# Optimization experiments

Hardware: AMD Instinct MI355X
Metric: run time of the kernel (lower is better)

Reference implementation:

```python
import jax, jax.numpy as jnp
import numpy as np

EPS = 1e-5


def setup_inputs() -> dict:
    key = jax.random.key(0)
    ks = jax.random.split(key, 14)
    N, C, H, W, D = 2048, 512, 4, 4, 64
    inp = {
        "x": jax.random.normal(ks[0], (N, C, H, W), jnp.float32),
        "W123": jax.random.normal(ks[1], (3, D, C), jnp.float32) * 0.05,
        "b123": jax.random.normal(ks[2], (3, D), jnp.float32) * 0.05,
        "g123": jax.random.uniform(ks[3], (3, D), jnp.float32, 0.5, 1.5),
        "be123": jax.random.normal(ks[4], (3, D), jnp.float32) * 0.05,
        "m123": jax.random.normal(ks[5], (3, D), jnp.float32) * 0.05,
        "v123": jax.random.uniform(ks[6], (3, D), jnp.float32, 0.5, 1.5),
        "W4": jax.random.normal(ks[7], (C, D), jnp.float32) * 0.05,
        "b4": jax.random.normal(ks[8], (C,), jnp.float32) * 0.05,
        "g4": jax.random.uniform(ks[9], (C,), jnp.float32, 0.5, 1.5),
        "be4": jax.random.normal(ks[10], (C,), jnp.float32) * 0.05,
        "m4": jax.random.normal(ks[11], (C,), jnp.float32) * 0.05,
        "v4": jax.random.uniform(ks[12], (C,), jnp.float32, 0.5, 1.5),
    }
    return inp


def reference(x, W123, b123, g123, be123, m123, v123, W4, b4, g4, be4, m4, v4):
    N, C, H, W = x.shape
    D = W123.shape[1]
    # three parallel 1x1 stride-2 conv branches == strided slice + channel GEMM
    xs = x[:, :, ::2, ::2]                                 # (N, C, H/2, W/2)
    proj = jnp.einsum('nchw,koc->knohw', xs, W123)         # (3, N, D, H/2, W/2)
    bcast = lambda p: p[:, None, :, None, None]
    bn = (proj + bcast(b123) - bcast(m123)) * (bcast(g123) / jnp.sqrt(bcast(v123) + EPS)) + bcast(be123)
    act = jax.nn.relu(bn)                                  # (3, N, D, h, w)
    L = act.shape[-2] * act.shape[-1]
    q = act[0].reshape(N, D, L).transpose(0, 2, 1)         # (N, L, D)
    k = act[1].reshape(N, D, L)                            # (N, D, L)
    v = act[2].reshape(N, D, L).transpose(0, 2, 1)         # (N, L, D)
    attn = jax.nn.softmax(jnp.einsum('nld,ndm->nlm', q, k), axis=2)  # (N, L, L)
    att = jnp.einsum('nlm,nmd->nld', attn, v).transpose(0, 2, 1)     # (N, D, L)
    att = att.reshape(N, D, W, -1)                         # (N, D, W, L//W)
    # conv2: 1x1 conv D->C + BN (no ReLU)
    out2 = jnp.einsum('ndhw,cd->nchw', att, W4) + b4[None, :, None, None]
    cb = lambda p: p[None, :, None, None]
    bn2 = (out2 - cb(m4)) * (cb(g4) / jnp.sqrt(cb(v4) + EPS)) + cb(be4)
    return x + bn2                                         # broadcasts (N,C,4,1) -> (N,C,4,4)
```

## Files before the change

kernel.cpp:

```cpp
#include <hip/hip_runtime.h>
#include <hip/hip_bf16.h>
#include <math.h>

#define EPS 1e-5f

typedef __attribute__((ext_vector_type(8))) short bf8_t;
typedef __attribute__((ext_vector_type(4))) float f4_t;

static __device__ __forceinline__ unsigned short f2b(float f) {
    __hip_bfloat16 h = __float2bfloat16(f);
    return *reinterpret_cast<unsigned short*>(&h);
}


__global__ __launch_bounds__(256) void k0_prep(
    const float* __restrict__ W123, const float* __restrict__ W4,
    const float* __restrict__ b123, const float* __restrict__ g123,
    const float* __restrict__ be123, const float* __restrict__ m123, const float* __restrict__ v123,
    const float* __restrict__ b4, const float* __restrict__ g4,
    const float* __restrict__ be4, const float* __restrict__ m4, const float* __restrict__ v4,
    unsigned short* __restrict__ w1b, unsigned short* __restrict__ w4b,
    float* __restrict__ bn1s, float* __restrict__ bn1h,
    float* __restrict__ bn2s, float* __restrict__ bn2h)
{
    const int bid = blockIdx.x, tid = threadIdx.x;
    if (bid == 64) {
        if (tid < 192) {
            float s = g123[tid] * rsqrtf(v123[tid] + EPS);
            bn1s[tid] = s;
            bn1h[tid] = be123[tid] + (b123[tid] - m123[tid]) * s;
        }
        for (int c = tid; c < 512; c += 256) {
            float s = g4[c] * rsqrtf(v4[c] + EPS);
            bn2s[c] = s;
            bn2h[c] = be4[c] + (b4[c] - m4[c]) * s;
        }
        return;
    }
    const int f = bid * 256 + tid;
    const float* src;
    unsigned short* dst;
    if (f < 12288) {
        int mt = f >> 10, ks = (f >> 6) & 15, lane = f & 63;
        int row = mt * 16 + (lane & 15);
        int k0  = ks * 32 + ((lane >> 4) << 3);
        src = W123 + row * 512 + k0;
        dst = w1b + f * 8;
    } else {
        int f2 = f - 12288;
        int mt = f2 >> 7, ks = (f2 >> 6) & 1, lane = f2 & 63;
        int row = mt * 16 + (lane & 15);
        int k0  = ks * 32 + ((lane >> 4) << 3);
        src = W4 + row * 64 + k0;
        dst = w4b + f2 * 8;
    }
    float4 a = *(const float4*)src;
    float4 b = *(const float4*)(src + 4);
    union { unsigned short u[8]; uint4 v; } o;
    o.u[0]=f2b(a.x); o.u[1]=f2b(a.y); o.u[2]=f2b(a.z); o.u[3]=f2b(a.w);
    o.u[4]=f2b(b.x); o.u[5]=f2b(b.y); o.u[6]=f2b(b.z); o.u[7]=f2b(b.w);
    *(uint4*)dst = o.v;
}

__global__ __launch_bounds__(256) void k1_mfma(
    const float* __restrict__ x,
    const unsigned short* __restrict__ w1b,
    const unsigned short* __restrict__ w4b,
    const float* __restrict__ bn1s, const float* __restrict__ bn1h,
    const float* __restrict__ bn2s, const float* __restrict__ bn2h,
    float* __restrict__ bn2g)
{
    __shared__ unsigned short Bxs[16][536];
    __shared__ float actL[192][17];
    __shared__ float smx[4][17];
    __shared__ unsigned short B2[16][72];
    __shared__ float C2T[16][524];

    const int tid = threadIdx.x;
    const int lane = tid & 63, w = tid >> 6;
    const int n0 = blockIdx.x * 4;

    #pragma unroll
    for (int it = 0; it < 8; ++it) {
        int i = it * 256 + tid;
        int s = i >> 9, c = i & 511;
        const float* xp = x + (size_t)(n0 + s) * 8192 + c * 16;
        float4 a = *(const float4*)xp;
        float4 b = *(const float4*)(xp + 8);
        Bxs[s * 4 + 0][c] = f2b(a.x);
        Bxs[s * 4 + 1][c] = f2b(a.z);
        Bxs[s * 4 + 2][c] = f2b(b.x);
        Bxs[s * 4 + 3][c] = f2b(b.z);
    }
    __syncthreads();

    {
        f4_t acc[3] = {};
        const bf8_t* Af = (const bf8_t*)w1b;
        const int col = lane & 15, kg = (lane >> 4) << 3;
        for (int ks = 0; ks < 16; ++ks) {
            bf8_t bf = *(const bf8_t*)&Bxs[col][ks * 32 + kg];
            #pragma unroll
            for (int mi = 0; mi < 3; ++mi) {
                int mt = w * 3 + mi;
                bf8_t af = Af[(mt * 16 + ks) * 64 + lane];
                acc[mi] = __builtin_amdgcn_mfma_f32_16x16x32_bf16(af, bf, acc[mi], 0, 0, 0);
            }
        }
        #pragma unroll
        for (int mi = 0; mi < 3; ++mi) {
            int rbase = (w * 3 + mi) * 16 + ((lane >> 4) << 2);
            #pragma unroll
            for (int r = 0; r < 4; ++r) {
                int row = rbase + r;
                float v = acc[mi][r] * bn1s[row] + bn1h[row];
                actL[row][col] = fmaxf(v, 0.f);
            }
        }
    }
    __syncthreads();

    if (tid < 128) {
        int s = tid >> 5, l = (tid >> 3) & 3, m = (tid >> 1) & 3, dg = tid & 1;
        float part = 0.f;
        #pragma unroll 8
        for (int k = 0; k < 32; ++k) {
            int d = dg * 32 + k;
            part += actL[d][s * 4 + l] * actL[64 + d][s * 4 + m];
        }
        part += __shfl_xor(part, 1);
        if (dg == 0) smx[s][l * 4 + m] = part;
    }
    __syncthreads();

    if (tid < 16) {
        int s = tid >> 2, l = tid & 3;
        float s0 = smx[s][l*4+0], s1 = smx[s][l*4+1], s2 = smx[s][l*4+2], s3 = smx[s][l*4+3];
        float mx = fmaxf(fmaxf(s0, s1), fmaxf(s2, s3));
        float e0 = expf(s0-mx), e1 = expf(s1-mx), e2 = expf(s2-mx), e3 = expf(s3-mx);
        float inv = 1.f / (e0 + e1 + e2 + e3);
        smx[s][l*4+0] = e0*inv; smx[s][l*4+1] = e1*inv;
        smx[s][l*4+2] = e2*inv; smx[s][l*4+3] = e3*inv;
    }
    __syncthreads();

    if (tid < 128) {
        int s = tid >> 5, l = (tid >> 3) & 3, d0 = (tid & 7) * 8;
        float p0 = smx[s][l*4+0], p1 = smx[s][l*4+1], p2 = smx[s][l*4+2], p3 = smx[s][l*4+3];
        #pragma unroll
        for (int j = 0; j < 8; ++j) {
            int d = d0 + j;
            float sum = p0 * actL[128+d][s*4+0] + p1 * actL[128+d][s*4+1]
                      + p2 * actL[128+d][s*4+2] + p3 * actL[128+d][s*4+3];
            B2[s * 4 + l][d] = f2b(sum);
        }
    }
    __syncthreads();

    {
        const bf8_t* A2f = (const bf8_t*)w4b;
        const int col = lane & 15, kg = (lane >> 4) << 3;
        f4_t acc2[8] = {};
        #pragma unroll
        for (int ks = 0; ks < 2; ++ks) {
            bf8_t bf = *(const bf8_t*)&B2[col][ks * 32 + kg];
            #pragma unroll
            for (int mi = 0; mi < 8; ++mi) {
                int mt = w * 8 + mi;
                bf8_t af = A2f[(mt * 2 + ks) * 64 + lane];
                acc2[mi] = __builtin_amdgcn_mfma_f32_16x16x32_bf16(af, bf, acc2[mi], 0, 0, 0);
            }
        }
        #pragma unroll
        for (int mi = 0; mi < 8; ++mi) {
            int cbase = (w * 8 + mi) * 16 + ((lane >> 4) << 2);
            #pragma unroll
            for (int r = 0; r < 4; ++r) {
                int c = cbase + r;
                C2T[col][c] = acc2[mi][r] * bn2s[c] + bn2h[c];
            }
        }
    }
    __syncthreads();

    #pragma unroll
    for (int it = 0; it < 8; ++it) {
        int j = it * 256 + tid;
        int s = j >> 9, c = j & 511;
        float4 v = make_float4(C2T[s*4+0][c], C2T[s*4+1][c], C2T[s*4+2][c], C2T[s*4+3][c]);
        *(float4*)(bn2g + (size_t)(n0 + s) * 2048 + c * 4) = v;
    }
}

__global__ __launch_bounds__(256) void k2_stream(
    const float* __restrict__ x,
    const float* __restrict__ bn2g,
    float* __restrict__ out)
{
    int i = blockIdx.x * 256 + threadIdx.x;
    #pragma unroll
    for (int it = 0; it < 8; ++it, i += 524288) {
        float4 xv = ((const float4*)x)[i];
        float b = bn2g[i];
        ((float4*)out)[i] = make_float4(xv.x + b, xv.y + b, xv.z + b, xv.w + b);
    }
}

extern "C" void kernel_launch(void* const* d_in, const int* in_sizes, int n_in,
                              void* d_out, int out_size, void* d_ws, size_t ws_size,
                              hipStream_t stream) {
    const float* x     = (const float*)d_in[0];
    const float* W123  = (const float*)d_in[1];
    const float* b123  = (const float*)d_in[2];
    const float* g123  = (const float*)d_in[3];
    const float* be123 = (const float*)d_in[4];
    const float* m123  = (const float*)d_in[5];
    const float* v123  = (const float*)d_in[6];
    const float* W4    = (const float*)d_in[7];
    const float* b4    = (const float*)d_in[8];
    const float* g4    = (const float*)d_in[9];
    const float* be4   = (const float*)d_in[10];
    const float* m4    = (const float*)d_in[11];
    const float* v4    = (const float*)d_in[12];
    float* outp = (float*)d_out;

    char* ws = (char*)d_ws;
    unsigned short* w1b = (unsigned short*)ws;
    unsigned short* w4b = (unsigned short*)(ws + 196608);
    float* bn1s = (float*)(ws + 262144);
    float* bn1h = (float*)(ws + 262912);
    float* bn2s = (float*)(ws + 263680);
    float* bn2h = (float*)(ws + 265728);
    float* bn2g = (float*)(ws + 524288);

    k0_prep<<<65, 256, 0, stream>>>(W123, W4, b123, g123, be123, m123, v123,
                                    b4, g4, be4, m4, v4,
                                    w1b, w4b, bn1s, bn1h, bn2s, bn2h);
    k1_mfma<<<512, 256, 0, stream>>>(x, w1b, w4b, bn1s, bn1h, bn2s, bn2h, bn2g);
    k2_stream<<<2048, 256, 0, stream>>>(x, bn2g, outp);
}
```

Before: 161.8 us.

## Fuse residual add into MFMA kernel and drop intermediate buffer and stream kernel

The final conv2+BN result is now added to x and written straight to the output inside the MFMA kernel. This removes the C2T shared-memory staging, the bn2g global round trip and the separate streaming kernel launch. The cost is that each thread's loads and stores are 16-byte accesses strided by 64 bytes across channels instead of fully contiguous, so coalescing is worse. It also re-reads x from global memory after it was loaded at kernel start.

```diff
diff --git a/kernel.cpp b/kernel.cpp
--- a/kernel.cpp
+++ b/kernel.cpp
@@ -68,13 +68,12 @@
     const unsigned short* __restrict__ w4b,
     const float* __restrict__ bn1s, const float* __restrict__ bn1h,
     const float* __restrict__ bn2s, const float* __restrict__ bn2h,
-    float* __restrict__ bn2g)
+    float* __restrict__ out)
 {
     __shared__ unsigned short Bxs[16][536];
     __shared__ float actL[192][17];
     __shared__ float smx[4][17];
     __shared__ unsigned short B2[16][72];
-    __shared__ float C2T[16][524];
 
     const int tid = threadIdx.x;
     const int lane = tid & 63, w = tid >> 6;
@@ -171,38 +170,20 @@
                 acc2[mi] = __builtin_amdgcn_mfma_f32_16x16x32_bf16(af, bf, acc2[mi], 0, 0, 0);
             }
         }
+        const int s = col >> 2, l = col & 3;
+        const float* xn = x + (size_t)(n0 + s) * 8192 + l * 4;
+        float* on = out + (size_t)(n0 + s) * 8192 + l * 4;
         #pragma unroll
         for (int mi = 0; mi < 8; ++mi) {
             int cbase = (w * 8 + mi) * 16 + ((lane >> 4) << 2);
             #pragma unroll
             for (int r = 0; r < 4; ++r) {
                 int c = cbase + r;
-                C2T[col][c] = acc2[mi][r] * bn2s[c] + bn2h[c];
-            }
-        }
-    }
-    __syncthreads();
-
-    #pragma unroll
-    for (int it = 0; it < 8; ++it) {
-        int j = it * 256 + tid;
-        int s = j >> 9, c = j & 511;
-        float4 v = make_float4(C2T[s*4+0][c], C2T[s*4+1][c], C2T[s*4+2][c], C2T[s*4+3][c]);
-        *(float4*)(bn2g + (size_t)(n0 + s) * 2048 + c * 4) = v;
-    }
-}
-
-__global__ __launch_bounds__(256) void k2_stream(
-    const float* __restrict__ x,
-    const float* __restrict__ bn2g,
-    float* __restrict__ out)
-{
-    int i = blockIdx.x * 256 + threadIdx.x;
-    #pragma unroll
-    for (int it = 0; it < 8; ++it, i += 524288) {
-        float4 xv = ((const float4*)x)[i];
-        float b = bn2g[i];
-        ((float4*)out)[i] = make_float4(xv.x + b, xv.y + b, xv.z + b, xv.w + b);
+                float b = acc2[mi][r] * bn2s[c] + bn2h[c];
+                float4 xv = *(const float4*)(xn + c * 16);
+                *(float4*)(on + c * 16) = make_float4(xv.x + b, xv.y + b, xv.z + b, xv.w + b);
+            }
+        }
     }
 }
 
@@ -231,11 +212,9 @@
     float* bn1h = (float*)(ws + 262912);
     float* bn2s = (float*)(ws + 263680);
     float* bn2h = (float*)(ws + 265728);
-    float* bn2g = (float*)(ws + 524288);
 
     k0_prep<<<65, 256, 0, stream>>>(W123, W4, b123, g123, be123, m123, v123,
                                     b4, g4, be4, m4, v4,
                                     w1b, w4b, bn1s, bn1h, bn2s, bn2h);
-    k1_mfma<<<512, 256, 0, stream>>>(x, w1b, w4b, bn1s, bn1h, bn2s, bn2h, bn2g);
-    k2_stream<<<2048, 256, 0, stream>>>(x, bn2g, outp);
-}
+    k1_mfma<<<512, 256, 0, stream>>>(x, w1b, w4b, bn1s, bn1h, bn2s, bn2h, outp);
+}
```

Measured after the change: 152.6 us. 1.06x faster.
